# Kernel optimization log

Measured on AMD Instinct MI355X. Metric: run time of the kernel, lower is better.

Reference implementation:

```python
import jax, jax.numpy as jnp
import numpy as np

N_NODES = 100000
N_EDGES = 1600000
NODES_PER_GRAPH = 100  # equal-sized graphs -> batch = arange // 100
POOL_K = 30


def setup_inputs() -> dict:
    key = jax.random.key(0)
    ks = jax.random.split(key, 8)
    F_IN, H1, H2, OUT = 128, 128, 128, 64
    x = jax.random.normal(ks[0], (N_NODES, F_IN), dtype=jnp.float32)
    edge_index = jax.random.randint(ks[1], (2, N_EDGES), 0, N_NODES, dtype=jnp.int64)
    batch = (jnp.arange(N_NODES, dtype=jnp.int64) // NODES_PER_GRAPH)
    # Glorot-ish init for weights, zero bias (as PyG GCNConv defaults)
    W1 = jax.random.normal(ks[2], (F_IN, H1), dtype=jnp.float32) / np.sqrt(F_IN)
    b1 = jnp.zeros((H1,), dtype=jnp.float32)
    W2 = jax.random.normal(ks[3], (H1, H2), dtype=jnp.float32) / np.sqrt(H1)
    b2 = jnp.zeros((H2,), dtype=jnp.float32)
    W3 = jax.random.normal(ks[4], (H2, OUT), dtype=jnp.float32) / np.sqrt(H2)
    b3 = jnp.zeros((OUT,), dtype=jnp.float32)
    return {"x": x, "edge_index": edge_index, "batch": batch,
            "W1": W1, "b1": b1, "W2": W2, "b2": b2, "W3": W3, "b3": b3}


def _gcn_conv(x, src, dst, W, b):
    """PyG GCNConv: xW, add self-loops, symmetric D^-1/2 A D^-1/2 scatter-add, +bias."""
    n = x.shape[0]
    loops = jnp.arange(n, dtype=src.dtype)
    row = jnp.concatenate([src, loops])  # message source
    col = jnp.concatenate([dst, loops])  # aggregation target
    xw = x @ W
    deg = jax.ops.segment_sum(jnp.ones(col.shape[0], x.dtype), col, num_segments=n)
    dinv = jnp.where(deg > 0, jax.lax.rsqrt(deg), 0.0)
    norm = dinv[row] * dinv[col]  # [E+N]
    out = jax.ops.segment_sum(xw[row] * norm[:, None], col, num_segments=n)
    return out + b


def _sort_pool(x, k):
    """global_sort_pool: per-graph descending sort by last channel, take top-k, flatten.
    Graphs are equal-sized and contiguous, so reshape to [B, P, C]."""
    n, c = x.shape
    xb = x.reshape(n // NODES_PER_GRAPH, NODES_PER_GRAPH, c)  # [B, P, C]
    order = jnp.argsort(-xb[..., -1], axis=1)[:, :k]          # [B, k]
    topk = jnp.take_along_axis(xb, order[..., None], axis=1)  # [B, k, C]
    return topk.reshape(topk.shape[0], k * c)


def reference(x, edge_index, batch, W1, b1, W2, b2, W3, b3):
    src, dst = edge_index[0], edge_index[1]
    h = jax.nn.relu(_gcn_conv(x, src, dst, W1, b1))
    h = jax.nn.relu(_gcn_conv(h, src, dst, W2, b2))
    h = _gcn_conv(h, src, dst, W3, b3)
    return _sort_pool(h, POOL_K)
```

## Files before the change

kernel.cpp:

```cpp
#include <hip/hip_runtime.h>
#include <math.h>

static inline size_t ws_align(size_t x) { return (x + 255) & ~(size_t)255; }

__global__ void count_kernel(const int* __restrict__ dst, int* __restrict__ counts, int E) {
  int e = blockIdx.x * 256 + threadIdx.x;
  if (e < E) atomicAdd(&counts[dst[e]], 1);
}

__global__ __launch_bounds__(256) void scanA_kernel(const int* __restrict__ counts,
    int* __restrict__ bsums, int n) {
  __shared__ int red[4];
  const int base = blockIdx.x * 1024;
  const int tid = threadIdx.x;
  int s = 0;
  #pragma unroll
  for (int u = 0; u < 4; ++u) {
    int i = base + u * 256 + tid;
    s += (i < n) ? counts[i] : 0;
  }
  #pragma unroll
  for (int m = 1; m < 64; m <<= 1) s += __shfl_xor(s, m, 64);
  if ((tid & 63) == 0) red[tid >> 6] = s;
  __syncthreads();
  if (tid == 0) bsums[blockIdx.x] = red[0] + red[1] + red[2] + red[3];
}

__global__ __launch_bounds__(128) void scanB_kernel(int* __restrict__ bsums, int nb) {
  __shared__ int tmp[129];
  int tid = threadIdx.x;
  tmp[tid] = (tid < nb) ? bsums[tid] : 0;
  __syncthreads();
  if (tid == 0) {
    int run = 0;
    for (int i = 0; i < nb; ++i) { int v = tmp[i]; tmp[i] = run; run += v; }
  }
  __syncthreads();
  if (tid < nb) bsums[tid] = tmp[tid];
}

__global__ __launch_bounds__(1024) void scanC_kernel(const int* __restrict__ counts,
    const int* __restrict__ bsums, int* __restrict__ offsets, int* __restrict__ cursor,
    double* __restrict__ dinv, int n) {
  __shared__ int warpsums[16];
  const int tid = threadIdx.x;
  const int lane = tid & 63, wid = tid >> 6;
  const int i = blockIdx.x * 1024 + tid;
  int v = (i < n) ? counts[i] : 0;
  int x = v;
  #pragma unroll
  for (int d = 1; d < 64; d <<= 1) {
    int y = __shfl_up(x, d, 64);
    if (lane >= d) x += y;
  }
  if (lane == 63) warpsums[wid] = x;
  __syncthreads();
  if (wid == 0) {
    int w = (lane < 16) ? warpsums[lane] : 0;
    #pragma unroll
    for (int d = 1; d < 16; d <<= 1) {
      int y = __shfl_up(w, d, 64);
      if (lane >= d) w += y;
    }
    if (lane < 16) warpsums[lane] = w;
  }
  __syncthreads();
  int excl = bsums[blockIdx.x] + x - v + (wid > 0 ? warpsums[wid - 1] : 0);
  if (i < n) {
    offsets[i] = excl;
    cursor[i] = excl;
    dinv[i] = 1.0 / sqrt((double)(v + 1));
    if (i == n - 1) offsets[n] = excl + v;
  }
}

__global__ void scatter_kernel(const int* __restrict__ src, const int* __restrict__ dst,
    int* __restrict__ cursor, int* __restrict__ srcs, float* __restrict__ ew,
    const double* __restrict__ dinv, int E, int use_ew) {
  int e = blockIdx.x * 256 + threadIdx.x;
  if (e < E) {
    int s = src[e], d = dst[e];
    int p = atomicAdd(&cursor[d], 1);
    srcs[p] = s;
    if (use_ew) ew[p] = (float)(dinv[s] * dinv[d]);
  }
}

template<int H>
__global__ __launch_bounds__(512, 4) void gemm_kernel(const float* __restrict__ X,
    const float* __restrict__ W, float* __restrict__ out, int N) {
  __shared__ float xs[128 * 68];
  const int tid  = threadIdx.x;
  const int row0 = blockIdx.x * 64;
  #pragma unroll
  for (int p = 0; p < 4; ++p) {
    int idx = p * 512 + tid;
    int r  = idx & 63;
    int c4 = idx >> 6;
    int grow = row0 + r;
    float4 v = make_float4(0.f, 0.f, 0.f, 0.f);
    if (grow < N) v = *(const float4*)(X + (size_t)grow * 128 + c4 * 4);
    float vals[4] = {v.x, v.y, v.z, v.w};
    #pragma unroll
    for (int j = 0; j < 4; ++j)
      xs[(4 * c4 + j) * 68 + r] = vals[j];
  }
  __syncthreads();
  constexpr int CPT = H / 32;
  const int rowg = tid & 15;
  const int colg = tid >> 4;
  const float* wbase = W + colg * CPT;

  double acc[4][CPT];
  #pragma unroll
  for (int j = 0; j < 4; ++j)
    #pragma unroll
    for (int h = 0; h < CPT; ++h) acc[j][h] = 0.0;

  float4 aA = *(const float4*)(xs + 4 * rowg);
  float4 aB;
  float bA[CPT], bB[CPT];
  #pragma unroll
  for (int h = 0; h < CPT; ++h) bA[h] = wbase[h];

  #pragma unroll 1
  for (int k = 0; k < 128; k += 2) {
    aB = *(const float4*)(xs + (k + 1) * 68 + 4 * rowg);
    #pragma unroll
    for (int h = 0; h < CPT; ++h) bB[h] = wbase[(size_t)(k + 1) * H + h];
    {
      double a0 = (double)aA.x, a1 = (double)aA.y, a2 = (double)aA.z, a3 = (double)aA.w;
      double b[CPT];
      #pragma unroll
      for (int h = 0; h < CPT; ++h) b[h] = (double)bA[h];
      #pragma unroll
      for (int h = 0; h < CPT; ++h) {
        acc[0][h] = fma(a0, b[h], acc[0][h]);
        acc[1][h] = fma(a1, b[h], acc[1][h]);
        acc[2][h] = fma(a2, b[h], acc[2][h]);
        acc[3][h] = fma(a3, b[h], acc[3][h]);
      }
    }
    if (k + 2 < 128) {
      aA = *(const float4*)(xs + (k + 2) * 68 + 4 * rowg);
      #pragma unroll
      for (int h = 0; h < CPT; ++h) bA[h] = wbase[(size_t)(k + 2) * H + h];
    }
    {
      double a0 = (double)aB.x, a1 = (double)aB.y, a2 = (double)aB.z, a3 = (double)aB.w;
      double b[CPT];
      #pragma unroll
      for (int h = 0; h < CPT; ++h) b[h] = (double)bB[h];
      #pragma unroll
      for (int h = 0; h < CPT; ++h) {
        acc[0][h] = fma(a0, b[h], acc[0][h]);
        acc[1][h] = fma(a1, b[h], acc[1][h]);
        acc[2][h] = fma(a2, b[h], acc[2][h]);
        acc[3][h] = fma(a3, b[h], acc[3][h]);
      }
    }
  }
  #pragma unroll
  for (int j = 0; j < 4; ++j) {
    int grow = row0 + rowg * 4 + j;
    if (grow < N) {
      float* o = out + (size_t)grow * H + colg * CPT;
      if constexpr (CPT == 4) {
        *(float4*)o = make_float4((float)acc[j][0], (float)acc[j][1],
                                  (float)acc[j][2], (float)acc[j][3]);
      } else {
        *(float2*)o = make_float2((float)acc[j][0], (float)acc[j][1]);
      }
    }
  }
}

template<int HOUT, bool USE_EW>
__global__ __launch_bounds__(512, 4) void fused_kernel(const float* __restrict__ xw_in,
    const double* __restrict__ dinv, const int* __restrict__ offs,
    const int* __restrict__ srcs, const float* __restrict__ ew,
    const float* __restrict__ bias, const float* __restrict__ Wn,
    float* __restrict__ xw_out, int N) {
  __shared__ float xs[128 * 68];
  const int tid  = threadIdx.x;
  const int wave = tid >> 6, lane = tid & 63;
  const int row0 = blockIdx.x * 64;
  const int grp  = lane >> 5;
  const int c0   = (lane & 31) * 4;

  for (int i = 0; i < 8; ++i) {
    const int n_loc = wave * 8 + i;
    const int node = row0 + n_loc;
    if (node >= N) break;
    const int e0 = offs[node], e1 = offs[node + 1];
    const double di = dinv[node];
    double a0 = 0.0, a1 = 0.0, a2 = 0.0, a3 = 0.0;
    for (int base = e0; base < e1; base += 16) {
      int ss[8]; double ww[8]; float4 vv[8];
      #pragma unroll
      for (int u = 0; u < 8; ++u) {
        int ee = base + u * 2 + grp;
        int cl = ee < e1 ? ee : e1 - 1;
        ss[u] = srcs[cl];
        if (USE_EW) ww[u] = (double)ew[cl];
      }
      #pragma unroll
      for (int u = 0; u < 8; ++u) {
        vv[u] = *(const float4*)(xw_in + (size_t)ss[u] * 128 + c0);
        if (!USE_EW) ww[u] = dinv[ss[u]];
      }
      #pragma unroll
      for (int u = 0; u < 8; ++u) {
        int ee = base + u * 2 + grp;
        double w = (ee < e1) ? ww[u] : 0.0;
        a0 = fma(w, (double)vv[u].x, a0);
        a1 = fma(w, (double)vv[u].y, a1);
        a2 = fma(w, (double)vv[u].z, a2);
        a3 = fma(w, (double)vv[u].w, a3);
      }
    }
    a0 += __shfl_xor(a0, 32, 64);
    a1 += __shfl_xor(a1, 32, 64);
    a2 += __shfl_xor(a2, 32, 64);
    a3 += __shfl_xor(a3, 32, 64);
    if (grp == 0) {
      const double d2 = di * di;
      float4 sv = *(const float4*)(xw_in + (size_t)node * 128 + c0);
      float4 bv = *(const float4*)(bias + c0);
      double o0, o1, o2, o3;
      if (USE_EW) {
        o0 = a0 + fma(d2, (double)sv.x, (double)bv.x);
        o1 = a1 + fma(d2, (double)sv.y, (double)bv.y);
        o2 = a2 + fma(d2, (double)sv.z, (double)bv.z);
        o3 = a3 + fma(d2, (double)sv.w, (double)bv.w);
      } else {
        o0 = fma(di, a0, fma(d2, (double)sv.x, (double)bv.x));
        o1 = fma(di, a1, fma(d2, (double)sv.y, (double)bv.y));
        o2 = fma(di, a2, fma(d2, (double)sv.z, (double)bv.z));
        o3 = fma(di, a3, fma(d2, (double)sv.w, (double)bv.w));
      }
      o0 = o0 > 0.0 ? o0 : 0.0; o1 = o1 > 0.0 ? o1 : 0.0;
      o2 = o2 > 0.0 ? o2 : 0.0; o3 = o3 > 0.0 ? o3 : 0.0;
      xs[(c0 + 0) * 68 + n_loc] = (float)o0;
      xs[(c0 + 1) * 68 + n_loc] = (float)o1;
      xs[(c0 + 2) * 68 + n_loc] = (float)o2;
      xs[(c0 + 3) * 68 + n_loc] = (float)o3;
    }
  }
  __syncthreads();

  constexpr int CPT = HOUT / 32;
  const int rowg = tid & 15;
  const int colg = tid >> 4;
  const float* wbase = Wn + colg * CPT;

  double acc[4][CPT];
  #pragma unroll
  for (int j = 0; j < 4; ++j)
    #pragma unroll
    for (int h = 0; h < CPT; ++h) acc[j][h] = 0.0;

  float4 aA = *(const float4*)(xs + 4 * rowg);
  float4 aB;
  float bA[CPT], bB[CPT];
  #pragma unroll
  for (int h = 0; h < CPT; ++h) bA[h] = wbase[h];

  #pragma unroll 1
  for (int k = 0; k < 128; k += 2) {
    aB = *(const float4*)(xs + (k + 1) * 68 + 4 * rowg);
    #pragma unroll
    for (int h = 0; h < CPT; ++h) bB[h] = wbase[(size_t)(k + 1) * HOUT + h];
    {
      double a0 = (double)aA.x, a1 = (double)aA.y, a2 = (double)aA.z, a3 = (double)aA.w;
      double b[CPT];
      #pragma unroll
      for (int h = 0; h < CPT; ++h) b[h] = (double)bA[h];
      #pragma unroll
      for (int h = 0; h < CPT; ++h) {
        acc[0][h] = fma(a0, b[h], acc[0][h]);
        acc[1][h] = fma(a1, b[h], acc[1][h]);
        acc[2][h] = fma(a2, b[h], acc[2][h]);
        acc[3][h] = fma(a3, b[h], acc[3][h]);
      }
    }
    if (k + 2 < 128) {
      aA = *(const float4*)(xs + (k + 2) * 68 + 4 * rowg);
      #pragma unroll
      for (int h = 0; h < CPT; ++h) bA[h] = wbase[(size_t)(k + 2) * HOUT + h];
    }
    {
      double a0 = (double)aB.x, a1 = (double)aB.y, a2 = (double)aB.z, a3 = (double)aB.w;
      double b[CPT];
      #pragma unroll
      for (int h = 0; h < CPT; ++h) b[h] = (double)bB[h];
      #pragma unroll
      for (int h = 0; h < CPT; ++h) {
        acc[0][h] = fma(a0, b[h], acc[0][h]);
        acc[1][h] = fma(a1, b[h], acc[1][h]);
        acc[2][h] = fma(a2, b[h], acc[2][h]);
        acc[3][h] = fma(a3, b[h], acc[3][h]);
      }
    }
  }
  #pragma unroll
  for (int j = 0; j < 4; ++j) {
    int grow = row0 + rowg * 4 + j;
    if (grow < N) {
      float* o = xw_out + (size_t)grow * HOUT + colg * CPT;
      if constexpr (CPT == 4) {
        *(float4*)o = make_float4((float)acc[j][0], (float)acc[j][1],
                                  (float)acc[j][2], (float)acc[j][3]);
      } else {
        *(float2*)o = make_float2((float)acc[j][0], (float)acc[j][1]);
      }
    }
  }
}

template<bool USE_EW>
__global__ __launch_bounds__(512, 2) void gather_pool_kernel(const float* __restrict__ xw,
    const double* __restrict__ dinv, const int* __restrict__ offs,
    const int* __restrict__ srcs, const float* __restrict__ ew,
    const float* __restrict__ bias, float* __restrict__ out, int N) {
  __shared__ float hl[100 * 64];
  __shared__ float sv[128];
  __shared__ int si[128];
  const int tid  = threadIdx.x;
  const int wave = tid >> 6, lane = tid & 63;
  const int g = blockIdx.x;
  const int grp = lane >> 4;
  const int c0  = (lane & 15) * 4;

  for (int n_loc = wave; n_loc < 100; n_loc += 8) {
    const int node = g * 100 + n_loc;
    const int e0 = offs[node], e1 = offs[node + 1];
    const double di = dinv[node];
    double a0 = 0.0, a1 = 0.0, a2 = 0.0, a3 = 0.0;
    for (int base = e0; base < e1; base += 16) {
      int ss[4]; double ww[4]; float4 vv[4];
      #pragma unroll
      for (int u = 0; u < 4; ++u) {
        int ee = base + u * 4 + grp;
        int cl = ee < e1 ? ee : e1 - 1;
        ss[u] = srcs[cl];
        if (USE_EW) ww[u] = (double)ew[cl];
      }
      #pragma unroll
      for (int u = 0; u < 4; ++u) {
        vv[u] = *(const float4*)(xw + (size_t)ss[u] * 64 + c0);
        if (!USE_EW) ww[u] = dinv[ss[u]];
      }
      #pragma unroll
      for (int u = 0; u < 4; ++u) {
        int ee = base + u * 4 + grp;
        double w = (ee < e1) ? ww[u] : 0.0;
        a0 = fma(w, (double)vv[u].x, a0);
        a1 = fma(w, (double)vv[u].y, a1);
        a2 = fma(w, (double)vv[u].z, a2);
        a3 = fma(w, (double)vv[u].w, a3);
      }
    }
    #pragma unroll
    for (int m = 16; m < 64; m <<= 1) {
      a0 += __shfl_xor(a0, m, 64);
      a1 += __shfl_xor(a1, m, 64);
      a2 += __shfl_xor(a2, m, 64);
      a3 += __shfl_xor(a3, m, 64);
    }
    if (grp == 0) {
      const double d2 = di * di;
      float4 svf = *(const float4*)(xw + (size_t)node * 64 + c0);
      float4 bv  = *(const float4*)(bias + c0);
      double o0, o1, o2, o3;
      if (USE_EW) {
        o0 = a0 + fma(d2, (double)svf.x, (double)bv.x);
        o1 = a1 + fma(d2, (double)svf.y, (double)bv.y);
        o2 = a2 + fma(d2, (double)svf.z, (double)bv.z);
        o3 = a3 + fma(d2, (double)svf.w, (double)bv.w);
      } else {
        o0 = fma(di, a0, fma(d2, (double)svf.x, (double)bv.x));
        o1 = fma(di, a1, fma(d2, (double)svf.y, (double)bv.y));
        o2 = fma(di, a2, fma(d2, (double)svf.z, (double)bv.z));
        o3 = fma(di, a3, fma(d2, (double)svf.w, (double)bv.w));
      }
      hl[n_loc * 64 + c0 + 0] = (float)o0;
      hl[n_loc * 64 + c0 + 1] = (float)o1;
      hl[n_loc * 64 + c0 + 2] = (float)o2;
      hl[n_loc * 64 + c0 + 3] = (float)o3;
    }
  }
  __syncthreads();
  if (tid < 128) {
    if (tid < 100) { sv[tid] = hl[tid * 64 + 63]; si[tid] = tid; }
    else           { sv[tid] = -3.0e38f;          si[tid] = 1 << 30; }
  }
  __syncthreads();
  for (int k = 2; k <= 128; k <<= 1) {
    for (int j = k >> 1; j > 0; j >>= 1) {
      if (tid < 128) {
        int l = tid ^ j;
        if (l > tid) {
          float va = sv[tid], vb = sv[l];
          int ia = si[tid], ib = si[l];
          bool a_before_b = (va > vb) || (va == vb && ia < ib);
          bool up = ((tid & k) == 0);
          bool sw = up ? !a_before_b : a_before_b;
          if (sw) { sv[tid] = vb; sv[l] = va; si[tid] = ib; si[l] = ia; }
        }
      }
      __syncthreads();
    }
  }
  for (int t = tid; t < 30 * 64; t += 512)
    out[(size_t)g * (30 * 64) + t] = hl[si[t >> 6] * 64 + (t & 63)];
}

extern "C" void kernel_launch(void* const* d_in, const int* in_sizes, int n_in,
                              void* d_out, int out_size, void* d_ws, size_t ws_size,
                              hipStream_t stream) {
  const float* x  = (const float*)d_in[0];
  const int*   ei = (const int*)d_in[1];
  const float* W1 = (const float*)d_in[3];
  const float* b1 = (const float*)d_in[4];
  const float* W2 = (const float*)d_in[5];
  const float* b2 = (const float*)d_in[6];
  const float* W3 = (const float*)d_in[7];
  const float* b3 = (const float*)d_in[8];

  const int N = in_sizes[0] / 128;
  const int E = in_sizes[1] / 2;
  const int* src = ei;
  const int* dst = ei + E;
  (void)n_in; (void)out_size;

  const int nb = (N + 1023) / 1024;

  char* ws = (char*)d_ws;
  size_t off = 0;
  auto alloc = [&](size_t bytes) { char* p = ws + off; off = ws_align(off + bytes); return p; };
  float*  xw      = (float*) alloc((size_t)N * 128 * 4);
  float*  h       = (float*) alloc((size_t)N * 128 * 4);
  double* dinv    = (double*)alloc((size_t)N * 8);
  int*    offsets = (int*)   alloc(((size_t)N + 1) * 4);
  int*    cursor  = (int*)   alloc((size_t)N * 4);
  int*    counts  = (int*)   alloc((size_t)N * 4);
  int*    srcs    = (int*)   alloc((size_t)E * 4);
  int*    bsums   = (int*)   alloc((size_t)(nb + 1) * 4);
  float*  ew      = (float*) alloc((size_t)E * 4);
  const bool use_ew = (off <= ws_size);

  hipMemsetAsync(counts, 0, (size_t)N * 4, stream);
  count_kernel<<<(E + 255) / 256, 256, 0, stream>>>(dst, counts, E);
  scanA_kernel<<<nb, 256, 0, stream>>>(counts, bsums, N);
  scanB_kernel<<<1, 128, 0, stream>>>(bsums, nb);
  scanC_kernel<<<nb, 1024, 0, stream>>>(counts, bsums, offsets, cursor, dinv, N);
  scatter_kernel<<<(E + 255) / 256, 256, 0, stream>>>(src, dst, cursor, srcs, ew, dinv, E, use_ew ? 1 : 0);

  const int gblocks = (N + 63) / 64;

  gemm_kernel<128><<<gblocks, 512, 0, stream>>>(x, W1, xw, N);
  if (use_ew) {
    fused_kernel<128, true ><<<gblocks, 512, 0, stream>>>(xw, dinv, offsets, srcs, ew, b1, W2, h, N);
    fused_kernel<64,  true ><<<gblocks, 512, 0, stream>>>(h,  dinv, offsets, srcs, ew, b2, W3, xw, N);
    gather_pool_kernel<true ><<<N / 100, 512, 0, stream>>>(xw, dinv, offsets, srcs, ew, b3, (float*)d_out, N);
  } else {
    fused_kernel<128, false><<<gblocks, 512, 0, stream>>>(xw, dinv, offsets, srcs, ew, b1, W2, h, N);
    fused_kernel<64,  false><<<gblocks, 512, 0, stream>>>(h,  dinv, offsets, srcs, ew, b2, W3, xw, N);
    gather_pool_kernel<false><<<N / 100, 512, 0, stream>>>(xw, dinv, offsets, srcs, ew, b3, (float*)d_out, N);
  }
}
```

Baseline: 847.2 us.

## Make fused GEMM per-wave to drop block barrier and transposed smem staging

Each wave now stores its 8 aggregated rows row-major in its own shared-memory slice and multiplies them by W itself, so the block-wide __syncthreads and transposed scatter stores go away. Each lane computes one row times HOUT/8 output columns with float4 loads of W. This removes cross-wave waiting between the gather and GEMM phases, but each W element is now read by every wave (more L1/global traffic) and per-thread accumulator count rises to 16 doubles, raising register pressure. Also, the gather loop breaks at N, so when N is not a multiple of 8 the tail lanes could read uninitialized rows, although their results are not written out.

```diff
diff --git a/kernel.cpp b/kernel.cpp
--- a/kernel.cpp
+++ b/kernel.cpp
@@ -181,16 +181,16 @@
     const int* __restrict__ srcs, const float* __restrict__ ew,
     const float* __restrict__ bias, const float* __restrict__ Wn,
     float* __restrict__ xw_out, int N) {
-  __shared__ float xs[128 * 68];
+  __shared__ float hs[8 * 8 * 132];
   const int tid  = threadIdx.x;
   const int wave = tid >> 6, lane = tid & 63;
   const int row0 = blockIdx.x * 64;
   const int grp  = lane >> 5;
   const int c0   = (lane & 31) * 4;
+  float* hrow = hs + wave * (8 * 132);
 
   for (int i = 0; i < 8; ++i) {
-    const int n_loc = wave * 8 + i;
-    const int node = row0 + n_loc;
+    const int node = row0 + wave * 8 + i;
     if (node >= N) break;
     const int e0 = offs[node], e1 = offs[node + 1];
     const double di = dinv[node];
@@ -241,80 +241,45 @@
       }
       o0 = o0 > 0.0 ? o0 : 0.0; o1 = o1 > 0.0 ? o1 : 0.0;
       o2 = o2 > 0.0 ? o2 : 0.0; o3 = o3 > 0.0 ? o3 : 0.0;
-      xs[(c0 + 0) * 68 + n_loc] = (float)o0;
-      xs[(c0 + 1) * 68 + n_loc] = (float)o1;
-      xs[(c0 + 2) * 68 + n_loc] = (float)o2;
-      xs[(c0 + 3) * 68 + n_loc] = (float)o3;
-    }
-  }
-  __syncthreads();
-
-  constexpr int CPT = HOUT / 32;
-  const int rowg = tid & 15;
-  const int colg = tid >> 4;
-  const float* wbase = Wn + colg * CPT;
-
-  double acc[4][CPT];
-  #pragma unroll
-  for (int j = 0; j < 4; ++j)
-    #pragma unroll
-    for (int h = 0; h < CPT; ++h) acc[j][h] = 0.0;
-
-  float4 aA = *(const float4*)(xs + 4 * rowg);
-  float4 aB;
-  float bA[CPT], bB[CPT];
-  #pragma unroll
-  for (int h = 0; h < CPT; ++h) bA[h] = wbase[h];
-
-  #pragma unroll 1
-  for (int k = 0; k < 128; k += 2) {
-    aB = *(const float4*)(xs + (k + 1) * 68 + 4 * rowg);
-    #pragma unroll
-    for (int h = 0; h < CPT; ++h) bB[h] = wbase[(size_t)(k + 1) * HOUT + h];
-    {
-      double a0 = (double)aA.x, a1 = (double)aA.y, a2 = (double)aA.z, a3 = (double)aA.w;
-      double b[CPT];
-      #pragma unroll
-      for (int h = 0; h < CPT; ++h) b[h] = (double)bA[h];
-      #pragma unroll
-      for (int h = 0; h < CPT; ++h) {
-        acc[0][h] = fma(a0, b[h], acc[0][h]);
-        acc[1][h] = fma(a1, b[h], acc[1][h]);
-        acc[2][h] = fma(a2, b[h], acc[2][h]);
-        acc[3][h] = fma(a3, b[h], acc[3][h]);
-      }
-    }
-    if (k + 2 < 128) {
-      aA = *(const float4*)(xs + (k + 2) * 68 + 4 * rowg);
-      #pragma unroll
-      for (int h = 0; h < CPT; ++h) bA[h] = wbase[(size_t)(k + 2) * HOUT + h];
-    }
-    {
-      double a0 = (double)aB.x, a1 = (double)aB.y, a2 = (double)aB.z, a3 = (double)aB.w;
-      double b[CPT];
-      #pragma unroll
-      for (int h = 0; h < CPT; ++h) b[h] = (double)bB[h];
-      #pragma unroll
-      for (int h = 0; h < CPT; ++h) {
-        acc[0][h] = fma(a0, b[h], acc[0][h]);
-        acc[1][h] = fma(a1, b[h], acc[1][h]);
-        acc[2][h] = fma(a2, b[h], acc[2][h]);
-        acc[3][h] = fma(a3, b[h], acc[3][h]);
-      }
-    }
-  }
-  #pragma unroll
-  for (int j = 0; j < 4; ++j) {
-    int grow = row0 + rowg * 4 + j;
-    if (grow < N) {
-      float* o = xw_out + (size_t)grow * HOUT + colg * CPT;
-      if constexpr (CPT == 4) {
-        *(float4*)o = make_float4((float)acc[j][0], (float)acc[j][1],
-                                  (float)acc[j][2], (float)acc[j][3]);
-      } else {
-        *(float2*)o = make_float2((float)acc[j][0], (float)acc[j][1]);
-      }
-    }
+      *(float4*)(hrow + i * 132 + c0) =
+          make_float4((float)o0, (float)o1, (float)o2, (float)o3);
+    }
+  }
+
+  constexpr int CW = HOUT / 8;
+  const int g  = lane >> 3;
+  const int c8 = lane & 7;
+  double acc[CW];
+  #pragma unroll
+  for (int h = 0; h < CW; ++h) acc[h] = 0.0;
+  const float* hp = hrow + g * 132;
+  const float* wb = Wn + c8 * CW;
+
+  #pragma unroll 2
+  for (int k = 0; k < 128; k += 4) {
+    float4 av = *(const float4*)(hp + k);
+    double aa[4];
+    aa[0] = (double)av.x; aa[1] = (double)av.y; aa[2] = (double)av.z; aa[3] = (double)av.w;
+    #pragma unroll
+    for (int kk = 0; kk < 4; ++kk) {
+      const float* wr = wb + (size_t)(k + kk) * HOUT;
+      #pragma unroll
+      for (int q = 0; q < CW / 4; ++q) {
+        float4 bv = *(const float4*)(wr + q * 4);
+        acc[q*4+0] = fma(aa[kk], (double)bv.x, acc[q*4+0]);
+        acc[q*4+1] = fma(aa[kk], (double)bv.y, acc[q*4+1]);
+        acc[q*4+2] = fma(aa[kk], (double)bv.z, acc[q*4+2]);
+        acc[q*4+3] = fma(aa[kk], (double)bv.w, acc[q*4+3]);
+      }
+    }
+  }
+  const int grow = row0 + wave * 8 + g;
+  if (grow < N) {
+    float* o = xw_out + (size_t)grow * HOUT + c8 * CW;
+    #pragma unroll
+    for (int q = 0; q < CW / 4; ++q)
+      *(float4*)(o + q * 4) = make_float4((float)acc[q*4+0], (float)acc[q*4+1],
+                                          (float)acc[q*4+2], (float)acc[q*4+3]);
   }
 }
 
```

New measurement: 1.145 ms. +35.2%, slower.
